# Kernel tuning notes

Hardware: AMD Instinct MI355X
Metric: run time of the kernel (lower is better)

Reference implementation:

```python
import jax, jax.numpy as jnp
import numpy as np

N_HEADS = 16

def setup_inputs() -> dict:
    key = jax.random.key(0)
    k1, k2, k3 = jax.random.split(key, 3)
    d = 1024
    x = jax.random.normal(k1, (4, 2048, d), dtype=jnp.float32)
    w_qkv = jax.random.normal(k2, (d, 3 * d), dtype=jnp.float32) * (1.0 / np.sqrt(d))
    w_proj = jax.random.normal(k3, (d, d), dtype=jnp.float32) * (1.0 / np.sqrt(d))
    return {"x": x, "w_qkv": w_qkv, "w_proj": w_proj}

def reference(x, w_qkv, w_proj):
    b, s, c = x.shape
    h = N_HEADS
    hd = c // h
    qkv = x @ w_qkv  # [b, s, 3c]
    q, k, v = jnp.split(qkv, 3, axis=-1)
    # [b, h, s, hd]
    q = q.reshape(b, s, h, hd).transpose(0, 2, 1, 3)
    k = k.reshape(b, s, h, hd).transpose(0, 2, 1, 3)
    v = v.reshape(b, s, h, hd).transpose(0, 2, 1, 3)
    scores = jnp.einsum('bhqd,bhkd->bhqk', q, k) / jnp.sqrt(jnp.float32(hd))
    causal = jnp.tril(jnp.ones((s, s), dtype=bool))
    scores = jnp.where(causal[None, None], scores, jnp.float32(-jnp.inf))
    attn = jax.nn.softmax(scores, axis=-1)
    out = jnp.einsum('bhqk,bhkd->bhqd', attn, v)
    out = out.transpose(0, 2, 1, 3).reshape(b, s, c)
    return out @ w_proj
```

## Files before the change

kernel.cpp:

```cpp
#include <hip/hip_runtime.h>
#include <hip/hip_bf16.h>

typedef unsigned short u16;
typedef __attribute__((ext_vector_type(8))) short short8;
typedef __attribute__((ext_vector_type(4))) float f32x4;
typedef __attribute__((ext_vector_type(16))) float f32x16;

__device__ inline u16 f2bf(float f) {
  unsigned u = __float_as_uint(f);
  u += 0x7fffu + ((u >> 16) & 1u);
  return (u16)(u >> 16);
}

__global__ __launch_bounds__(256) void cast_kernel(const float* __restrict__ in,
                                                   u16* __restrict__ out, int n4) {
  int i = blockIdx.x * 256 + threadIdx.x;
  if (i >= n4) return;
  float4 v = ((const float4*)in)[i];
  ushort4 o;
  o.x = f2bf(v.x); o.y = f2bf(v.y); o.z = f2bf(v.z); o.w = f2bf(v.w);
  ((ushort4*)out)[i] = o;
}

__global__ __launch_bounds__(256) void tcast_kernel(const float* __restrict__ in,
                                                    u16* __restrict__ out, int K, int N) {
  __shared__ float tile[32][33];
  int bx = blockIdx.x * 32;
  int by = blockIdx.y * 32;
  int tx = threadIdx.x & 31, ty = threadIdx.x >> 5;
#pragma unroll
  for (int i = 0; i < 4; i++) {
    int r = ty + i * 8;
    tile[r][tx] = in[(size_t)(by + r) * N + bx + tx];
  }
  __syncthreads();
#pragma unroll
  for (int i = 0; i < 4; i++) {
    int r = ty + i * 8;
    out[(size_t)(bx + r) * K + by + tx] = f2bf(tile[tx][r]);
  }
}

__global__ __launch_bounds__(256) void pack_kv(const u16* __restrict__ kbuf,
                                               const u16* __restrict__ vbuf,
                                               u16* __restrict__ kpack,
                                               u16* __restrict__ vpack) {
  __shared__ __align__(16) u16 ktile[64 * 72];
  __shared__ __align__(16) u16 vtile[64 * 72];
  int t = threadIdx.x;
  int kt = blockIdx.x, h = blockIdx.y, b = blockIdx.z;
  int bh = b * 16 + h;
  size_t rb = (size_t)(b * 2048 + kt * 64);
#pragma unroll
  for (int i = 0; i < 2; i++) {
    int idx = i * 256 + t; int r = idx >> 3, c8 = (idx & 7) * 8;
    *(uint4*)&ktile[r * 72 + c8] = *(const uint4*)(kbuf + (rb + r) * 1024 + h * 64 + c8);
    *(uint4*)&vtile[r * 72 + c8] = *(const uint4*)(vbuf + (rb + r) * 1024 + h * 64 + c8);
  }
  __syncthreads();
  u16* kd = kpack + ((size_t)bh * 32 + kt) * 4096;
  u16* vd = vpack + ((size_t)bh * 32 + kt) * 4096;
#pragma unroll
  for (int i = 0; i < 2; i++) {
    int idx = i * 256 + t;
    int j = idx >> 6, lane = idx & 63, l31 = lane & 31, hi5 = lane >> 5;
    *(uint4*)(kd + j * 512 + lane * 8) =
        *(const uint4*)&ktile[((j >> 2) * 32 + l31) * 72 + (j & 3) * 16 + hi5 * 8];
    union { u16 s[8]; uint4 u; } pv;
#pragma unroll
    for (int e = 0; e < 8; e++)
      pv.s[e] = vtile[((j & 3) * 16 + hi5 * 8 + e) * 72 + (j >> 2) * 32 + l31];
    *(uint4*)(vd + j * 512 + lane * 8) = pv.u;
  }
}


#define VMWAIT(n) asm volatile("s_waitcnt vmcnt(" #n ")" ::: "memory")
#define LGKM0()                                              \
  do {                                                       \
    asm volatile("s_waitcnt lgkmcnt(0)" ::: "memory");       \
    __builtin_amdgcn_sched_barrier(0);                       \
  } while (0)
#define BAR() asm volatile("s_barrier" ::: "memory")

__device__ __forceinline__ void gll16(const u16* g, u16* l) {
  __builtin_amdgcn_global_load_lds((const __attribute__((address_space(1))) unsigned*)g,
                                   (__attribute__((address_space(3))) unsigned*)l, 16, 0, 0);
}

__global__ __launch_bounds__(512, 2) void gemm_qkv(const u16* __restrict__ A,
                                                   const u16* __restrict__ Bt,
                                                   u16* __restrict__ qb,
                                                   u16* __restrict__ kb,
                                                   u16* __restrict__ vb) {
  __shared__ u16 lds[65536];
  int tid = threadIdx.x;
  int w = tid >> 6, lane = tid & 63, l15 = lane & 15, quad = lane >> 4;
  int wr = w >> 2, wc = w & 3;

  int bid = blockIdx.x;
  int wgid = (bid & 7) * 48 + (bid >> 3);
  int bm = (wgid / 12) * 256;
  int bn3 = (wgid % 12) * 256;

  int stc0 = w * 2, stc1 = w * 2 + 1;
  int srow = lane >> 2;
  int kswz = ((lane & 3) * 8) ^ ((lane >> 5) << 4);
  const u16* gA0 = A + (size_t)(bm + stc0 * 16 + srow) * 1024 + kswz;
  const u16* gA1 = A + (size_t)(bm + stc1 * 16 + srow) * 1024 + kswz;
  const u16* gB0 = Bt + (size_t)(bn3 + stc0 * 16 + srow) * 1024 + kswz;
  const u16* gB1 = Bt + (size_t)(bn3 + stc1 * 16 + srow) * 1024 + kswz;
  int dA0 = stc0 * 512, dA1 = stc1 * 512;

  int kq = (quad * 8) ^ ((l15 & 8) << 1);
  int aoffB = wr * 4096 + l15 * 32 + kq;
  int boffB = 8192 + wc * 2048 + l15 * 32 + kq;

  f32x4 acc[8][4];
#pragma unroll
  for (int m = 0; m < 8; m++)
#pragma unroll
    for (int n = 0; n < 4; n++) acc[m][n] = (f32x4)0.0f;

  short8 a0[4], a1[4], bb0[4], bb1[4];

#define STAGE_A(t)                                     \
  do {                                                 \
    u16* s_ = lds + ((t) & 3) * 16384;                 \
    gll16(gA0 + (t) * 32, s_ + dA0);                   \
    gll16(gA1 + (t) * 32, s_ + dA1);                   \
  } while (0)
#define STAGE_B(t)                                     \
  do {                                                 \
    u16* s_ = lds + ((t) & 3) * 16384 + 8192;          \
    gll16(gB0 + (t) * 32, s_ + dA0);                   \
    gll16(gB1 + (t) * 32, s_ + dA1);                   \
  } while (0)

#define PHASE_A(t, bbcur, DOSTG, VMN)                                                          \
  do {                                                                                         \
    const u16* sl = lds + ((t) & 3) * 16384;                                                   \
    _Pragma("unroll") for (int m = 0; m < 4; m++)                                              \
        a1[m] = *(const short8*)(sl + aoffB + (m + 4) * 512);                                  \
    if (DOSTG) STAGE_B((t) + 3);                                                               \
    BAR();                                                                                     \
    LGKM0();                                                                                   \
    __builtin_amdgcn_s_setprio(1);                                                             \
    _Pragma("unroll") for (int m = 0; m < 4; m++) _Pragma("unroll") for (int n = 0; n < 4; n++) \
        acc[m][n] = __builtin_amdgcn_mfma_f32_16x16x32_bf16(a0[m], bbcur[n], acc[m][n], 0, 0, 0); \
    __builtin_amdgcn_s_setprio(0);                                                             \
    VMN;                                                                                       \
    BAR();                                                                                     \
  } while (0)

#define PHASE_B(t, bbcur, bbnxt, DORD, DOSTG)                                                  \
  do {                                                                                         \
    if (DORD) {                                                                                \
      const u16* sl = lds + (((t) + 1) & 3) * 16384;                                           \
      _Pragma("unroll") for (int n = 0; n < 4; n++)                                            \
          bbnxt[n] = *(const short8*)(sl + boffB + n * 512);                                   \
      _Pragma("unroll") for (int m = 0; m < 4; m++)                                            \
          a0[m] = *(const short8*)(sl + aoffB + m * 512);                                      \
    }                                                                                          \
    if (DOSTG) STAGE_A((t) + 4);                                                               \
    BAR();                                                                                     \
    LGKM0();                                                                                   \
    __builtin_amdgcn_s_setprio(1);                                                             \
    _Pragma("unroll") for (int m = 0; m < 4; m++) _Pragma("unroll") for (int n = 0; n < 4; n++) \
        acc[m + 4][n] =                                                                        \
            __builtin_amdgcn_mfma_f32_16x16x32_bf16(a1[m], bbcur[n], acc[m + 4][n], 0, 0, 0);  \
    __builtin_amdgcn_s_setprio(0);                                                             \
    BAR();                                                                                     \
  } while (0)

  STAGE_A(0); STAGE_B(0); STAGE_A(1); STAGE_B(1); STAGE_A(2); STAGE_B(2); STAGE_A(3);
  VMWAIT(10);
  BAR();
  {
    const u16* sl = lds;
#pragma unroll
    for (int n = 0; n < 4; n++) bb0[n] = *(const short8*)(sl + boffB + n * 512);
#pragma unroll
    for (int m = 0; m < 4; m++) a0[m] = *(const short8*)(sl + aoffB + m * 512);
  }

  for (int t = 0; t < 28; t += 2) {
    PHASE_A(t, bb0, 1, VMWAIT(8));
    PHASE_B(t, bb0, bb1, 1, 1);
    PHASE_A(t + 1, bb1, 1, VMWAIT(8));
    PHASE_B(t + 1, bb1, bb0, 1, 1);
  }
  PHASE_A(28, bb0, 1, VMWAIT(8));
  PHASE_B(28, bb0, bb1, 1, 0);
  PHASE_A(29, bb1, 0, VMWAIT(4));
  PHASE_B(29, bb1, bb0, 1, 0);
  PHASE_A(30, bb0, 0, VMWAIT(0));
  PHASE_B(30, bb0, bb1, 1, 0);
  PHASE_A(31, bb1, 0, );
  PHASE_B(31, bb1, bb0, 0, 0);

#undef PHASE_A
#undef PHASE_B
#undef STAGE_A
#undef STAGE_B

  u16* dst = (bn3 < 1024) ? qb : (bn3 < 2048) ? kb : vb;
  float scl = (bn3 < 1024) ? 0.18033688011112f : 1.0f;
  int bnl = bn3 & 1023;
  int rbase = bm + wr * 128 + quad * 4;
  int cbase = bnl + wc * 64 + l15;
#pragma unroll
  for (int m = 0; m < 8; m++)
#pragma unroll
    for (int n = 0; n < 4; n++)
#pragma unroll
      for (int r = 0; r < 4; r++)
        dst[(size_t)(rbase + m * 16 + r) * 1024 + cbase + n * 16] = f2bf(acc[m][n][r] * scl);
}

#define GEMM_BODY(KSTR)                                                                       \
  __shared__ __align__(16) u16 As[128 * 32];                                                  \
  __shared__ __align__(16) u16 Bs[128 * 32];                                                  \
  int t = threadIdx.x;                                                                        \
  int wave = t >> 6, lane = t & 63, l15 = lane & 15, quad = lane >> 4;                        \
  int bn = blockIdx.x * 128, bm = blockIdx.y * 128;                                           \
  int wm = (wave >> 1) * 64, wn = (wave & 1) * 64;                                            \
  f32x4 acc[4][4];                                                                            \
  for (int i = 0; i < 4; i++)                                                                 \
    for (int j = 0; j < 4; j++) acc[i][j] = (f32x4)0.0f;                                      \
  int srow = wave * 16 + (lane >> 2);                                                         \
  int scol = (lane & 3) * 8;                                                                  \
  const u16* ga0 = A + (size_t)(bm + srow) * KSTR + scol;                                     \
  const u16* ga1 = A + (size_t)(bm + 64 + srow) * KSTR + scol;                                \
  const u16* gb0 = Bt + (size_t)(bn + srow) * KSTR + scol;                                    \
  const u16* gb1 = Bt + (size_t)(bn + 64 + srow) * KSTR + scol;                               \
  u16* lA0 = As + wave * 512;                                                                 \
  u16* lA1 = As + 2048 + wave * 512;                                                          \
  u16* lB0 = Bs + wave * 512;                                                                 \
  u16* lB1 = Bs + 2048 + wave * 512;                                                          \
  for (int k0 = 0; k0 < KSTR; k0 += 32) {                                                     \
    __syncthreads();                                                                          \
    __builtin_amdgcn_global_load_lds((const __attribute__((address_space(1))) unsigned*)(ga0 + k0), \
                                     (__attribute__((address_space(3))) unsigned*)lA0, 16, 0, 0);   \
    __builtin_amdgcn_global_load_lds((const __attribute__((address_space(1))) unsigned*)(ga1 + k0), \
                                     (__attribute__((address_space(3))) unsigned*)lA1, 16, 0, 0);   \
    __builtin_amdgcn_global_load_lds((const __attribute__((address_space(1))) unsigned*)(gb0 + k0), \
                                     (__attribute__((address_space(3))) unsigned*)lB0, 16, 0, 0);   \
    __builtin_amdgcn_global_load_lds((const __attribute__((address_space(1))) unsigned*)(gb1 + k0), \
                                     (__attribute__((address_space(3))) unsigned*)lB1, 16, 0, 0);   \
    __syncthreads();                                                                          \
    short8 a[4], b[4];                                                                        \
    for (int mt = 0; mt < 4; mt++)                                                            \
      a[mt] = *(const short8*)(&As[(wm + mt * 16 + l15) * 32 + quad * 8]);                    \
    for (int nt = 0; nt < 4; nt++)                                                            \
      b[nt] = *(const short8*)(&Bs[(wn + nt * 16 + l15) * 32 + quad * 8]);                    \
    for (int mt = 0; mt < 4; mt++)                                                            \
      for (int nt = 0; nt < 4; nt++)                                                          \
        acc[mt][nt] = __builtin_amdgcn_mfma_f32_16x16x32_bf16(a[mt], b[nt], acc[mt][nt], 0, 0, 0); \
  }

__global__ __launch_bounds__(256) void gemm_proj(const u16* __restrict__ A,
                                                 const u16* __restrict__ Bt,
                                                 float* __restrict__ Co) {
  GEMM_BODY(1024)
#pragma unroll
  for (int mt = 0; mt < 4; mt++)
#pragma unroll
    for (int nt = 0; nt < 4; nt++)
#pragma unroll
      for (int r = 0; r < 4; r++) {
        int row = bm + wm + mt * 16 + quad * 4 + r;
        int col = bn + wn + nt * 16 + l15;
        Co[(size_t)row * 1024 + col] = acc[mt][nt][r];
      }
}

__global__ __launch_bounds__(256, 2) void attn_kernel(const u16* __restrict__ qbuf,
                                                      const u16* __restrict__ kpack,
                                                      const u16* __restrict__ vpack,
                                                      u16* __restrict__ ctx) {
  int t = threadIdx.x;
  int wave = t >> 6, lane = t & 63, l31 = lane & 31, hi = lane >> 5;
  int bh = blockIdx.x;
  int s = (int)blockIdx.y * 4 + wave;
  int b = bh >> 4, h = bh & 15;
  int rowbase = b * 2048;
  int hi4 = hi * 4;

  const u16* kp = kpack + (size_t)bh * (32 * 4096) + lane * 8;
  const u16* vp = vpack + (size_t)bh * (32 * 4096) + lane * 8;

#pragma unroll
  for (int ph = 0; ph < 2; ph++) {
    int strip = ph ? 63 - s : s;
    int q0 = strip * 32;
    int q_lane = q0 + l31;

    const u16* qp = qbuf + (size_t)(rowbase + q_lane) * 1024 + h * 64 + hi * 8;
    short8 qf[4];
#pragma unroll
    for (int ks = 0; ks < 4; ks++) qf[ks] = *(const short8*)(qp + ks * 16);

    float l_run = 0.0f;
    f32x16 o[2];
    o[0] = (f32x16)0.0f; o[1] = (f32x16)0.0f;
    int ktmax = (q0 + 31) >> 6;

    for (int kt = 0; kt <= ktmax; kt++) {
      const u16* kb = kp + kt * 4096;
      const u16* vb = vp + kt * 4096;

      short8 ka[8], vv[8];
#pragma unroll
      for (int j = 0; j < 8; j++) {
        ka[j] = *(const short8*)(kb + j * 512);
        vv[j] = *(const short8*)(vb + j * 512);
      }

      f32x16 st0 = (f32x16)0.0f, st1 = (f32x16)0.0f;
#pragma unroll
      for (int ks = 0; ks < 4; ks++) {
        st0 = __builtin_amdgcn_mfma_f32_32x32x16_bf16(ka[ks], qf[ks], st0, 0, 0, 0);
        st1 = __builtin_amdgcn_mfma_f32_32x32x16_bf16(ka[4 + ks], qf[ks], st1, 0, 0, 0);
      }

      unsigned pk[2][8];
      if (kt == ktmax) {
#pragma unroll
        for (int ii = 0; ii < 8; ii++) {
          int key = kt * 64 + ((2 * ii) & 3) + 8 * ((2 * ii) >> 2) + hi4;
          float p00 = (key     <= q_lane) ? __builtin_amdgcn_exp2f(st0[2 * ii])     : 0.0f;
          float p01 = (key + 1 <= q_lane) ? __builtin_amdgcn_exp2f(st0[2 * ii + 1]) : 0.0f;
          float p10 = (key + 32 <= q_lane) ? __builtin_amdgcn_exp2f(st1[2 * ii])     : 0.0f;
          float p11 = (key + 33 <= q_lane) ? __builtin_amdgcn_exp2f(st1[2 * ii + 1]) : 0.0f;
          l_run += p00 + p01 + p10 + p11;
          pk[0][ii] = ((__float_as_uint(p00) + 0x8000u) >> 16) |
                      ((__float_as_uint(p01) + 0x8000u) & 0xffff0000u);
          pk[1][ii] = ((__float_as_uint(p10) + 0x8000u) >> 16) |
                      ((__float_as_uint(p11) + 0x8000u) & 0xffff0000u);
        }
      } else {
#pragma unroll
        for (int ii = 0; ii < 8; ii++) {
          float p00 = __builtin_amdgcn_exp2f(st0[2 * ii]);
          float p01 = __builtin_amdgcn_exp2f(st0[2 * ii + 1]);
          float p10 = __builtin_amdgcn_exp2f(st1[2 * ii]);
          float p11 = __builtin_amdgcn_exp2f(st1[2 * ii + 1]);
          l_run += p00 + p01 + p10 + p11;
          pk[0][ii] = ((__float_as_uint(p00) + 0x8000u) >> 16) |
                      ((__float_as_uint(p01) + 0x8000u) & 0xffff0000u);
          pk[1][ii] = ((__float_as_uint(p10) + 0x8000u) >> 16) |
                      ((__float_as_uint(p11) + 0x8000u) & 0xffff0000u);
        }
      }

      short8 pf[4];
#pragma unroll
      for (int ks2 = 0; ks2 < 4; ks2++) {
        int km = ks2 >> 1, h4 = (ks2 & 1) * 4;
        unsigned A0 = pk[km][h4 + 0], A1 = pk[km][h4 + 1];
        unsigned B0 = pk[km][h4 + 2], B1 = pk[km][h4 + 3];
        unsigned tA0 = (unsigned)__shfl_xor((int)A0, 32);
        unsigned tA1 = (unsigned)__shfl_xor((int)A1, 32);
        unsigned tB0 = (unsigned)__shfl_xor((int)B0, 32);
        unsigned tB1 = (unsigned)__shfl_xor((int)B1, 32);
        union { unsigned u[4]; short8 sh; } fr;
        fr.u[0] = hi ? tB0 : A0;
        fr.u[1] = hi ? tB1 : A1;
        fr.u[2] = hi ? B0 : tA0;
        fr.u[3] = hi ? B1 : tA1;
        pf[ks2] = fr.sh;
      }

#pragma unroll
      for (int am = 0; am < 2; am++)
#pragma unroll
        for (int ks2 = 0; ks2 < 4; ks2++)
          o[am] = __builtin_amdgcn_mfma_f32_32x32x16_bf16(vv[am * 4 + ks2], pf[ks2], o[am], 0, 0, 0);
    }

    float l_tot = l_run + __shfl_xor(l_run, 32);
    float inv = 1.0f / l_tot;
    size_t obase = (size_t)(rowbase + q_lane) * 1024 + h * 64;
#pragma unroll
    for (int am = 0; am < 2; am++)
#pragma unroll
      for (int k = 0; k < 4; k++) {
        ushort4 w;
        w.x = f2bf(o[am][4 * k + 0] * inv);
        w.y = f2bf(o[am][4 * k + 1] * inv);
        w.z = f2bf(o[am][4 * k + 2] * inv);
        w.w = f2bf(o[am][4 * k + 3] * inv);
        *(ushort4*)&ctx[obase + am * 32 + k * 8 + hi4] = w;
      }
  }
}

extern "C" void kernel_launch(void* const* d_in, const int* in_sizes, int n_in,
                              void* d_out, int out_size, void* d_ws, size_t ws_size,
                              hipStream_t stream) {
  const float* x      = (const float*)d_in[0];
  const float* w_qkv  = (const float*)d_in[1];
  const float* w_proj = (const float*)d_in[2];
  float* out = (float*)d_out;

  char* ws = (char*)d_ws;
  const size_t MB = 1024 * 1024;
  u16* qbuf   = (u16*)(ws);
  u16* kbuf   = (u16*)(ws + 16 * MB);
  u16* vbuf   = (u16*)(ws + 32 * MB);
  u16* xb     = (u16*)(ws + 48 * MB);
  u16* kpack  = (u16*)(ws + 48 * MB);
  u16* vpack  = (u16*)(ws + 64 * MB);
  u16* wqkvT  = (u16*)(ws + 80 * MB);
  u16* wprojT = (u16*)(ws + 86 * MB);
  u16* ctx    = kbuf;

  cast_kernel<<<8192, 256, 0, stream>>>(x, xb, 2097152);
  tcast_kernel<<<dim3(96, 32), 256, 0, stream>>>(w_qkv, wqkvT, 1024, 3072);
  tcast_kernel<<<dim3(32, 32), 256, 0, stream>>>(w_proj, wprojT, 1024, 1024);

  gemm_qkv<<<dim3(384), 512, 0, stream>>>(xb, wqkvT, qbuf, kbuf, vbuf);
  pack_kv<<<dim3(32, 16, 4), 256, 0, stream>>>(kbuf, vbuf, kpack, vpack);
  attn_kernel<<<dim3(64, 8), 256, 0, stream>>>(qbuf, kpack, vpack, ctx);
  gemm_proj<<<dim3(8, 64), 256, 0, stream>>>(ctx, wprojT, out);
}
```

Measured before the change: 258.2 us.

## Split LDS fragment prefetch across phases with partial lgkmcnt waits in QKV GEMM

Reworks the QKV GEMM software pipeline so the next B fragments are read from LDS half in phase A and half in phase B. Both phases now wait only for earlier LDS reads (lgkmcnt(6)), so the freshly issued reads overlap the current MFMA block instead of draining first. The vmcnt waits move from phase A to phase B, with adjusted counts for the prologue and tail. This aims to hide LDS read latency behind matrix work, at the cost of more fragile counter-based ordering that relies on LDS ops completing in order.

```diff
diff --git a/kernel.cpp b/kernel.cpp
--- a/kernel.cpp
+++ b/kernel.cpp
@@ -76,9 +76,9 @@
 
 
 #define VMWAIT(n) asm volatile("s_waitcnt vmcnt(" #n ")" ::: "memory")
-#define LGKM0()                                              \
+#define LGKM(n)                                              \
   do {                                                       \
-    asm volatile("s_waitcnt lgkmcnt(0)" ::: "memory");       \
+    asm volatile("s_waitcnt lgkmcnt(" #n ")" ::: "memory");  \
     __builtin_amdgcn_sched_barrier(0);                       \
   } while (0)
 #define BAR() asm volatile("s_barrier" ::: "memory")
@@ -137,44 +137,49 @@
     gll16(gB1 + (t) * 32, s_ + dA1);                   \
   } while (0)
 
-#define PHASE_A(t, bbcur, DOSTG, VMN)                                                          \
+#define PHASE_A(t, cur, nxt, DONXT, DOSTG)                                                     \
   do {                                                                                         \
-    const u16* sl = lds + ((t) & 3) * 16384;                                                   \
+    const u16* slA = lds + ((t) & 3) * 16384;                                                  \
+    const u16* slN = lds + (((t) + 1) & 3) * 16384;                                            \
     _Pragma("unroll") for (int m = 0; m < 4; m++)                                              \
-        a1[m] = *(const short8*)(sl + aoffB + (m + 4) * 512);                                  \
+        a1[m] = *(const short8*)(slA + aoffB + (m + 4) * 512);                                 \
+    if (DONXT) {                                                                               \
+      nxt[0] = *(const short8*)(slN + boffB + 0 * 512);                                        \
+      nxt[1] = *(const short8*)(slN + boffB + 1 * 512);                                        \
+    }                                                                                          \
     if (DOSTG) STAGE_B((t) + 3);                                                               \
     BAR();                                                                                     \
-    LGKM0();                                                                                   \
+    LGKM(6);                                                                                   \
     __builtin_amdgcn_s_setprio(1);                                                             \
     _Pragma("unroll") for (int m = 0; m < 4; m++) _Pragma("unroll") for (int n = 0; n < 4; n++) \
-        acc[m][n] = __builtin_amdgcn_mfma_f32_16x16x32_bf16(a0[m], bbcur[n], acc[m][n], 0, 0, 0); \
+        acc[m][n] = __builtin_amdgcn_mfma_f32_16x16x32_bf16(a0[m], cur[n], acc[m][n], 0, 0, 0); \
+    __builtin_amdgcn_s_setprio(0);                                                             \
+    BAR();                                                                                     \
+  } while (0)
+
+#define PHASE_B(t, cur, nxt, DORD, DOSTG, WN, VMN)                                             \
+  do {                                                                                         \
+    if (DORD) {                                                                                \
+      const u16* slN = lds + (((t) + 1) & 3) * 16384;                                          \
+      nxt[2] = *(const short8*)(slN + boffB + 2 * 512);                                        \
+      nxt[3] = *(const short8*)(slN + boffB + 3 * 512);                                        \
+      _Pragma("unroll") for (int m = 0; m < 4; m++)                                            \
+          a0[m] = *(const short8*)(slN + aoffB + m * 512);                                     \
+    }                                                                                          \
+    if (DOSTG) STAGE_A((t) + 4);                                                               \
+    BAR();                                                                                     \
+    LGKM(WN);                                                                                  \
+    __builtin_amdgcn_s_setprio(1);                                                             \
+    _Pragma("unroll") for (int m = 0; m < 4; m++) _Pragma("unroll") for (int n = 0; n < 4; n++) \
+        acc[m + 4][n] =                                                                        \
+            __builtin_amdgcn_mfma_f32_16x16x32_bf16(a1[m], cur[n], acc[m + 4][n], 0, 0, 0);    \
     __builtin_amdgcn_s_setprio(0);                                                             \
     VMN;                                                                                       \
     BAR();                                                                                     \
   } while (0)
 
-#define PHASE_B(t, bbcur, bbnxt, DORD, DOSTG)                                                  \
-  do {                                                                                         \
-    if (DORD) {                                                                                \
-      const u16* sl = lds + (((t) + 1) & 3) * 16384;                                           \
-      _Pragma("unroll") for (int n = 0; n < 4; n++)                                            \
-          bbnxt[n] = *(const short8*)(sl + boffB + n * 512);                                   \
-      _Pragma("unroll") for (int m = 0; m < 4; m++)                                            \
-          a0[m] = *(const short8*)(sl + aoffB + m * 512);                                      \
-    }                                                                                          \
-    if (DOSTG) STAGE_A((t) + 4);                                                               \
-    BAR();                                                                                     \
-    LGKM0();                                                                                   \
-    __builtin_amdgcn_s_setprio(1);                                                             \
-    _Pragma("unroll") for (int m = 0; m < 4; m++) _Pragma("unroll") for (int n = 0; n < 4; n++) \
-        acc[m + 4][n] =                                                                        \
-            __builtin_amdgcn_mfma_f32_16x16x32_bf16(a1[m], bbcur[n], acc[m + 4][n], 0, 0, 0);  \
-    __builtin_amdgcn_s_setprio(0);                                                             \
-    BAR();                                                                                     \
-  } while (0)
-
   STAGE_A(0); STAGE_B(0); STAGE_A(1); STAGE_B(1); STAGE_A(2); STAGE_B(2); STAGE_A(3);
-  VMWAIT(10);
+  VMWAIT(6);
   BAR();
   {
     const u16* sl = lds;
@@ -185,19 +190,19 @@
   }
 
   for (int t = 0; t < 28; t += 2) {
-    PHASE_A(t, bb0, 1, VMWAIT(8));
-    PHASE_B(t, bb0, bb1, 1, 1);
-    PHASE_A(t + 1, bb1, 1, VMWAIT(8));
-    PHASE_B(t + 1, bb1, bb0, 1, 1);
-  }
-  PHASE_A(28, bb0, 1, VMWAIT(8));
-  PHASE_B(28, bb0, bb1, 1, 0);
-  PHASE_A(29, bb1, 0, VMWAIT(4));
-  PHASE_B(29, bb1, bb0, 1, 0);
-  PHASE_A(30, bb0, 0, VMWAIT(0));
-  PHASE_B(30, bb0, bb1, 1, 0);
-  PHASE_A(31, bb1, 0, );
-  PHASE_B(31, bb1, bb0, 0, 0);
+    PHASE_A(t, bb0, bb1, 1, 1);
+    PHASE_B(t, bb0, bb1, 1, 1, 6, VMWAIT(6));
+    PHASE_A(t + 1, bb1, bb0, 1, 1);
+    PHASE_B(t + 1, bb1, bb0, 1, 1, 6, VMWAIT(6));
+  }
+  PHASE_A(28, bb0, bb1, 1, 1);
+  PHASE_B(28, bb0, bb1, 1, 0, 6, VMWAIT(4));
+  PHASE_A(29, bb1, bb0, 1, 0);
+  PHASE_B(29, bb1, bb0, 1, 0, 6, VMWAIT(0));
+  PHASE_A(30, bb0, bb1, 1, 0);
+  PHASE_B(30, bb0, bb1, 1, 0, 6, (void)0);
+  PHASE_A(31, bb1, bb0, 0, 0);
+  PHASE_B(31, bb1, bb0, 0, 0, 0, (void)0);
 
 #undef PHASE_A
 #undef PHASE_B
```

New measurement: 258.0 us. About the same (-0.1%).

## Restructure QKV GEMM pipeline to 64-wide K tiles with split half-tile staging

Applied to the files above, without the earlier changes.

The QKV projection GEMM now stages 64-wide K slices in a double-buffered LDS layout instead of a four-deep ring of 32-wide slices, and splits each tile into A and B halves. The main loop becomes four phases that each run 16 MFMAs across all 8 M-subtiles while prefetching the next half-tile. This halves the number of loop iterations and barriers per K step and reuses each A fragment across two B fragments. The cost is a different register footprint (8 A fragments held at once) and less prefetch depth for the B operand.

```diff
diff --git a/kernel.cpp b/kernel.cpp
--- a/kernel.cpp
+++ b/kernel.cpp
@@ -103,18 +103,16 @@
   int bm = (wgid / 12) * 256;
   int bn3 = (wgid % 12) * 256;
 
-  int stc0 = w * 2, stc1 = w * 2 + 1;
   int srow = lane >> 2;
   int kswz = ((lane & 3) * 8) ^ ((lane >> 5) << 4);
-  const u16* gA0 = A + (size_t)(bm + stc0 * 16 + srow) * 1024 + kswz;
-  const u16* gA1 = A + (size_t)(bm + stc1 * 16 + srow) * 1024 + kswz;
-  const u16* gB0 = Bt + (size_t)(bn3 + stc0 * 16 + srow) * 1024 + kswz;
-  const u16* gB1 = Bt + (size_t)(bn3 + stc1 * 16 + srow) * 1024 + kswz;
-  int dA0 = stc0 * 512, dA1 = stc1 * 512;
+  const u16* gA0 = A + (size_t)(bm + w * 16 + srow) * 1024 + kswz;
+  const u16* gA1 = A + (size_t)(bm + 128 + w * 16 + srow) * 1024 + kswz;
+  const u16* gB0 = Bt + (size_t)(bn3 + w * 16 + srow) * 1024 + kswz;
+  const u16* gB1 = Bt + (size_t)(bn3 + 128 + w * 16 + srow) * 1024 + kswz;
 
   int kq = (quad * 8) ^ ((l15 & 8) << 1);
-  int aoffB = wr * 4096 + l15 * 32 + kq;
-  int boffB = 8192 + wc * 2048 + l15 * 32 + kq;
+  int aoff = wr * 8192 + l15 * 32 + kq;
+  int boff = 16384 + (wc >> 1) * 8192 + (wc & 1) * 2048 + l15 * 32 + kq;
 
   f32x4 acc[8][4];
 #pragma unroll
@@ -122,87 +120,125 @@
 #pragma unroll
     for (int n = 0; n < 4; n++) acc[m][n] = (f32x4)0.0f;
 
-  short8 a0[4], a1[4], bb0[4], bb1[4];
-
-#define STAGE_A(t)                                     \
-  do {                                                 \
-    u16* s_ = lds + ((t) & 3) * 16384;                 \
-    gll16(gA0 + (t) * 32, s_ + dA0);                   \
-    gll16(gA1 + (t) * 32, s_ + dA1);                   \
-  } while (0)
-#define STAGE_B(t)                                     \
-  do {                                                 \
-    u16* s_ = lds + ((t) & 3) * 16384 + 8192;          \
-    gll16(gB0 + (t) * 32, s_ + dA0);                   \
-    gll16(gB1 + (t) * 32, s_ + dA1);                   \
-  } while (0)
-
-#define PHASE_A(t, bbcur, DOSTG, VMN)                                                          \
+  short8 a[8], bA[4], bB[4];
+
+#define STAGE_AH0(T)                                          \
+  do {                                                        \
+    u16* d_ = lds + ((T) & 1) * 32768 + w * 512;              \
+    gll16(gA0 + (size_t)(T) * 64, d_);                        \
+    gll16(gA0 + (size_t)(T) * 64 + 32, d_ + 4096);            \
+  } while (0)
+#define STAGE_AH1(T)                                          \
+  do {                                                        \
+    u16* d_ = lds + ((T) & 1) * 32768 + 8192 + w * 512;       \
+    gll16(gA1 + (size_t)(T) * 64, d_);                        \
+    gll16(gA1 + (size_t)(T) * 64 + 32, d_ + 4096);            \
+  } while (0)
+#define STAGE_BH0(T)                                          \
+  do {                                                        \
+    u16* d_ = lds + ((T) & 1) * 32768 + 16384 + w * 512;      \
+    gll16(gB0 + (size_t)(T) * 64, d_);                        \
+    gll16(gB0 + (size_t)(T) * 64 + 32, d_ + 4096);            \
+  } while (0)
+#define STAGE_BH1(T)                                          \
+  do {                                                        \
+    u16* d_ = lds + ((T) & 1) * 32768 + 24576 + w * 512;      \
+    gll16(gB1 + (size_t)(T) * 64, d_);                        \
+    gll16(gB1 + (size_t)(T) * 64 + 32, d_ + 4096);            \
+  } while (0)
+
+#define MFMA16(NLO, BV0, BV1)                                                                  \
   do {                                                                                         \
-    const u16* sl = lds + ((t) & 3) * 16384;                                                   \
-    _Pragma("unroll") for (int m = 0; m < 4; m++)                                              \
-        a1[m] = *(const short8*)(sl + aoffB + (m + 4) * 512);                                  \
-    if (DOSTG) STAGE_B((t) + 3);                                                               \
+    __builtin_amdgcn_s_setprio(1);                                                             \
+    _Pragma("unroll") for (int m = 0; m < 8; m++)                                              \
+        acc[m][NLO] = __builtin_amdgcn_mfma_f32_16x16x32_bf16(a[m], BV0, acc[m][NLO], 0, 0, 0);\
+    _Pragma("unroll") for (int m = 0; m < 8; m++)                                              \
+        acc[m][NLO + 1] =                                                                      \
+            __builtin_amdgcn_mfma_f32_16x16x32_bf16(a[m], BV1, acc[m][NLO + 1], 0, 0, 0);      \
+    __builtin_amdgcn_s_setprio(0);                                                             \
+  } while (0)
+
+#define PHASE1(T, DOSTG)                                                                       \
+  do {                                                                                         \
+    const u16* bc_ = lds + ((T) & 1) * 32768;                                                  \
+    _Pragma("unroll") for (int m = 0; m < 8; m++)                                              \
+        a[m] = *(const short8*)(bc_ + aoff + m * 512);                                         \
+    if (DOSTG) STAGE_AH0((T) + 1);                                                             \
+    BAR(); LGKM0();                                                                            \
+    MFMA16(0, bA[0], bA[1]);                                                                   \
     BAR();                                                                                     \
-    LGKM0();                                                                                   \
-    __builtin_amdgcn_s_setprio(1);                                                             \
-    _Pragma("unroll") for (int m = 0; m < 4; m++) _Pragma("unroll") for (int n = 0; n < 4; n++) \
-        acc[m][n] = __builtin_amdgcn_mfma_f32_16x16x32_bf16(a0[m], bbcur[n], acc[m][n], 0, 0, 0); \
-    __builtin_amdgcn_s_setprio(0);                                                             \
+  } while (0)
+
+#define PHASE2(T, DOSTG)                                                                       \
+  do {                                                                                         \
+    const u16* bc_ = lds + ((T) & 1) * 32768;                                                  \
+    _Pragma("unroll") for (int n = 0; n < 4; n++)                                              \
+        bB[n] = *(const short8*)(bc_ + boff + 4096 + n * 512);                                 \
+    if (DOSTG) STAGE_AH1((T) + 1);                                                             \
+    BAR(); LGKM0();                                                                            \
+    MFMA16(2, bA[2], bA[3]);                                                                   \
+    BAR();                                                                                     \
+  } while (0)
+
+#define PHASE3(T, DOSTG, VMN)                                                                  \
+  do {                                                                                         \
+    const u16* bc_ = lds + ((T) & 1) * 32768;                                                  \
+    _Pragma("unroll") for (int m = 0; m < 8; m++)                                              \
+        a[m] = *(const short8*)(bc_ + aoff + 4096 + m * 512);                                  \
+    if (DOSTG) STAGE_BH0((T) + 2);                                                             \
+    BAR(); LGKM0();                                                                            \
+    MFMA16(0, bB[0], bB[1]);                                                                   \
     VMN;                                                                                       \
     BAR();                                                                                     \
   } while (0)
 
-#define PHASE_B(t, bbcur, bbnxt, DORD, DOSTG)                                                  \
+#define PHASE4(T, DORD, DOSTG, VMN)                                                            \
   do {                                                                                         \
     if (DORD) {                                                                                \
-      const u16* sl = lds + (((t) + 1) & 3) * 16384;                                           \
+      const u16* bn_ = lds + (((T) + 1) & 1) * 32768;                                          \
       _Pragma("unroll") for (int n = 0; n < 4; n++)                                            \
-          bbnxt[n] = *(const short8*)(sl + boffB + n * 512);                                   \
-      _Pragma("unroll") for (int m = 0; m < 4; m++)                                            \
-          a0[m] = *(const short8*)(sl + aoffB + m * 512);                                      \
+          bA[n] = *(const short8*)(bn_ + boff + n * 512);                                      \
     }                                                                                          \
-    if (DOSTG) STAGE_A((t) + 4);                                                               \
+    if (DOSTG) STAGE_BH1((T) + 2);                                                             \
+    BAR(); LGKM0();                                                                            \
+    MFMA16(2, bB[2], bB[3]);                                                                   \
+    VMN;                                                                                       \
     BAR();                                                                                     \
-    LGKM0();                                                                                   \
-    __builtin_amdgcn_s_setprio(1);                                                             \
-    _Pragma("unroll") for (int m = 0; m < 4; m++) _Pragma("unroll") for (int n = 0; n < 4; n++) \
-        acc[m + 4][n] =                                                                        \
-            __builtin_amdgcn_mfma_f32_16x16x32_bf16(a1[m], bbcur[n], acc[m + 4][n], 0, 0, 0);  \
-    __builtin_amdgcn_s_setprio(0);                                                             \
-    BAR();                                                                                     \
-  } while (0)
-
-  STAGE_A(0); STAGE_B(0); STAGE_A(1); STAGE_B(1); STAGE_A(2); STAGE_B(2); STAGE_A(3);
-  VMWAIT(10);
+  } while (0)
+
+  STAGE_BH0(0); STAGE_BH1(0); STAGE_AH0(0); STAGE_AH1(0); STAGE_BH0(1); STAGE_BH1(1);
+  VMWAIT(4);
   BAR();
   {
-    const u16* sl = lds;
-#pragma unroll
-    for (int n = 0; n < 4; n++) bb0[n] = *(const short8*)(sl + boffB + n * 512);
-#pragma unroll
-    for (int m = 0; m < 4; m++) a0[m] = *(const short8*)(sl + aoffB + m * 512);
-  }
-
-  for (int t = 0; t < 28; t += 2) {
-    PHASE_A(t, bb0, 1, VMWAIT(8));
-    PHASE_B(t, bb0, bb1, 1, 1);
-    PHASE_A(t + 1, bb1, 1, VMWAIT(8));
-    PHASE_B(t + 1, bb1, bb0, 1, 1);
-  }
-  PHASE_A(28, bb0, 1, VMWAIT(8));
-  PHASE_B(28, bb0, bb1, 1, 0);
-  PHASE_A(29, bb1, 0, VMWAIT(4));
-  PHASE_B(29, bb1, bb0, 1, 0);
-  PHASE_A(30, bb0, 0, VMWAIT(0));
-  PHASE_B(30, bb0, bb1, 1, 0);
-  PHASE_A(31, bb1, 0, );
-  PHASE_B(31, bb1, bb0, 0, 0);
-
-#undef PHASE_A
-#undef PHASE_B
-#undef STAGE_A
-#undef STAGE_B
+    const u16* bc_ = lds;
+#pragma unroll
+    for (int n = 0; n < 4; n++) bA[n] = *(const short8*)(bc_ + boff + n * 512);
+  }
+
+  for (int T = 0; T < 14; ++T) {
+    PHASE1(T, 1);
+    PHASE2(T, 1);
+    PHASE3(T, 1, VMWAIT(6));
+    PHASE4(T, 1, 1, VMWAIT(4));
+  }
+  PHASE1(14, 1);
+  PHASE2(14, 1);
+  PHASE3(14, 0, VMWAIT(4));
+  PHASE4(14, 1, 0, VMWAIT(0));
+  PHASE1(15, 0);
+  PHASE2(15, 0);
+  PHASE3(15, 0, (void)0);
+  PHASE4(15, 0, 0, (void)0);
+
+#undef PHASE1
+#undef PHASE2
+#undef PHASE3
+#undef PHASE4
+#undef MFMA16
+#undef STAGE_AH0
+#undef STAGE_AH1
+#undef STAGE_BH0
+#undef STAGE_BH1
 
   u16* dst = (bn3 < 1024) ? qb : (bn3 < 2048) ? kb : vb;
   float scl = (bn3 < 1024) ? 0.18033688011112f : 1.0f;
```

New measurement: 254.4 us. Within noise of the previous version (-1.5%).
